# Kernel tuning notes

Measured on AMD Instinct MI355X. Metric: run time of the kernel, lower is better.

## Reference

```python
import jax, jax.numpy as jnp
import numpy as np

SEQ, B, I, H = 512, 64, 1024, 1024

def setup_inputs() -> dict:
    key = jax.random.key(0)
    ks = jax.random.split(key, 6)
    scale_ih = 1.0 / np.sqrt(I)
    scale_hh = 1.0 / np.sqrt(H)
    return {
        "input": jax.random.normal(ks[0], (SEQ, B, I), dtype=jnp.float32),
        "h_0": jax.random.normal(ks[1], (1, B, H), dtype=jnp.float32),
        "weight_ih": jax.random.normal(ks[2], (3 * H, I), dtype=jnp.float32) * scale_ih,
        "weight_hh": jax.random.normal(ks[3], (3 * H, H), dtype=jnp.float32) * scale_hh,
        "bias_ih": jax.random.normal(ks[4], (3 * H,), dtype=jnp.float32) * scale_hh,
        "bias_hh": jax.random.normal(ks[5], (3 * H,), dtype=jnp.float32) * scale_hh,
    }


def _gru_lbr0(input, h0, weight_ih, weight_hh, bias_ih, bias_hh):
    """Unidirectional GRU, ONNX linear_before_reset=0 semantics.

    r_t = sigmoid(x W_ir^T + b_ir + h W_hr^T + b_hr)
    z_t = sigmoid(x W_iz^T + b_iz + h W_hz^T + b_hz)
    n_t = tanh(x W_in^T + b_in + (r_t * h) W_hn^T + b_hn)
    h_t = (1 - z_t) * n_t + z_t * h
    """
    hidden = h0.shape[-1]
    # Precompute all input projections in one big GEMM: (S, B, 3H)
    gx = jnp.einsum('sbi,gi->sbg', input, weight_ih) + bias_ih
    W_hr, W_hz, W_hn = jnp.split(weight_hh, 3, axis=0)
    b_hr, b_hz, b_hn = jnp.split(bias_hh, 3, axis=0)

    def step(h, gx_t):
        gx_r, gx_z, gx_n = jnp.split(gx_t, 3, axis=-1)
        r = jax.nn.sigmoid(gx_r + h @ W_hr.T + b_hr)
        z = jax.nn.sigmoid(gx_z + h @ W_hz.T + b_hz)
        n = jnp.tanh(gx_n + (r * h) @ W_hn.T + b_hn)
        h_new = (1.0 - z) * n + z * h
        return h_new, h_new

    h_n, outputs = jax.lax.scan(step, h0, gx)
    return outputs, h_n  # (S, B, H), (B, H)


def reference(input, h_0, weight_ih, weight_hh, bias_ih, bias_hh):
    seq_len, batch, _ = input.shape
    hidden = weight_hh.shape[1]
    outputs, h_n = _gru_lbr0(input, h_0[0], weight_ih, weight_hh, bias_ih, bias_hh)
    # Match GRUWrapper output layout: Y = (S, num_dir=1, B, H), Y_h = (1, B, H)
    Y = outputs.reshape(seq_len, batch, 1, hidden).transpose(0, 2, 1, 3)
    Y_h = h_n[None, :, :]
    return (Y, Y_h)
```

## Files before the change

### kernel.cpp

```cpp
#include <hip/hip_runtime.h>

typedef unsigned short ushort_t;
typedef short sh8 __attribute__((ext_vector_type(8)));
typedef float f32x4 __attribute__((ext_vector_type(4)));

#define MFMA16(a,b,c) __builtin_amdgcn_mfma_f32_16x16x32_bf16((a),(b),(c),0,0,0)

#define SEQL   512
#define BATCH  64
#define HDIM   1024
#define G3     3072
#define AROWS  (SEQL*BATCH)
#define YSZ    (SEQL*BATCH*HDIM)
#define BH     (BATCH*HDIM)
#define NWG    64
#define NGEMM  192
#define NTILE  768

#define TILES_TOTAL (256*24)
#define TILES_PER_WG (TILES_TOTAL/NGEMM)

__device__ __forceinline__ ushort_t f2bf(float x) {
  unsigned u = __float_as_uint(x);
  u += 0x7FFFu + ((u >> 16) & 1u);
  return (ushort_t)(u >> 16);
}
__device__ __forceinline__ float bf2f(ushort_t h) {
  return __uint_as_float(((unsigned)h) << 16);
}

__global__ void cvt_kernel(const float* __restrict__ wih, const float* __restrict__ whh,
                           const float* __restrict__ h0,
                           ushort_t* __restrict__ WihH, ushort_t* __restrict__ WihL,
                           ushort_t* __restrict__ WhhH, ushort_t* __restrict__ WhhL,
                           ushort_t* __restrict__ hH) {
  const int NW = G3 * HDIM;
  int i0 = blockIdx.x * blockDim.x + threadIdx.x;
  int stride = gridDim.x * blockDim.x;
  for (int i = i0; i < NW; i += stride) {
    float x = wih[i]; ushort_t h = f2bf(x);
    WihH[i] = h; WihL[i] = f2bf(x - bf2f(h));
    float y = whh[i]; ushort_t g = f2bf(y);
    WhhH[i] = g; WhhL[i] = f2bf(y - bf2f(g));
  }
  for (int i = i0; i < BH; i += stride) {
    hH[i] = f2bf(h0[i]);
  }
}

__device__ __forceinline__ void gbar_flat(unsigned* slots, int g, int tid, unsigned e) {
  __syncthreads();
  if (tid < 64) {
    if (tid == 0)
      __hip_atomic_store(slots + g * 32, e, __ATOMIC_RELEASE, __HIP_MEMORY_SCOPE_AGENT);
    unsigned* sp = slots + tid * 32;
    while (__hip_atomic_load(sp, __ATOMIC_RELAXED, __HIP_MEMORY_SCOPE_AGENT) < e)
      __builtin_amdgcn_s_sleep(1);
    (void)__hip_atomic_load(sp, __ATOMIC_ACQUIRE, __HIP_MEMORY_SCOPE_AGENT);
  }
  __syncthreads();
}

__global__ __launch_bounds__(256, 1) void mega(
    const float* __restrict__ A,
    const ushort_t* __restrict__ WihH, const ushort_t* __restrict__ WihL,
    const float* __restrict__ bih,
    float* __restrict__ gx,
    const ushort_t* __restrict__ WhhH, const ushort_t* __restrict__ WhhL,
    const float* __restrict__ bhh,
    const float* __restrict__ h0f,
    ushort_t* __restrict__ hH,
    ushort_t* __restrict__ rhH,
    float* __restrict__ Y, float* __restrict__ Yh,
    unsigned* __restrict__ slots,
    unsigned* __restrict__ prog)
{
  extern __shared__ char lds[];
  const int g = blockIdx.x;
  const int tid = threadIdx.x;
  const int w = tid >> 6, l = tid & 63;
  const int lr = l & 15, lk = (l >> 4) * 8, rb = (l >> 4) * 4;

  if (g >= NWG) {
    const int base = g - NWG;
    for (int kk = 0; kk < TILES_PER_WG; ++kk) {
      int tile = base + NGEMM * kk;
      int mt = tile / 24, nt = tile % 24;

      f32x4 acc[2][8];
      #pragma unroll
      for (int mi = 0; mi < 2; ++mi)
        #pragma unroll
        for (int ni = 0; ni < 8; ++ni) acc[mi][ni] = (f32x4){0.f, 0.f, 0.f, 0.f};

      int arow0 = mt * 128 + w * 32 + lr;
      int brow0 = nt * 128 + lr;

      for (int k0 = 0; k0 < HDIM; k0 += 32) {
        int ka = k0 + lk;
        sh8 aH[2], aL[2];
        #pragma unroll
        for (int mi = 0; mi < 2; ++mi) {
          const float* ap = A + (size_t)(arow0 + mi * 16) * HDIM + ka;
          float4 x0 = *(const float4*)ap;
          float4 x1 = *(const float4*)(ap + 4);
          float xs[8] = {x0.x, x0.y, x0.z, x0.w, x1.x, x1.y, x1.z, x1.w};
          #pragma unroll
          for (int j = 0; j < 8; ++j) {
            ushort_t h = f2bf(xs[j]);
            aH[mi][j] = (short)h;
            aL[mi][j] = (short)f2bf(xs[j] - bf2f(h));
          }
        }
        #pragma unroll
        for (int ni = 0; ni < 8; ++ni) {
          const ushort_t* bh = WihH + (size_t)(brow0 + ni * 16) * HDIM + ka;
          const ushort_t* bl = WihL + (size_t)(brow0 + ni * 16) * HDIM + ka;
          sh8 bHf = *(const sh8*)bh;
          sh8 bLf = *(const sh8*)bl;
          #pragma unroll
          for (int mi = 0; mi < 2; ++mi) {
            acc[mi][ni] = MFMA16(aH[mi], bHf, acc[mi][ni]);
            acc[mi][ni] = MFMA16(aH[mi], bLf, acc[mi][ni]);
            acc[mi][ni] = MFMA16(aL[mi], bHf, acc[mi][ni]);
          }
        }
      }
      int rbq = (l >> 4) * 4;
      #pragma unroll
      for (int mi = 0; mi < 2; ++mi)
        #pragma unroll
        for (int ni = 0; ni < 8; ++ni) {
          int col = nt * 128 + ni * 16 + lr;
          float b = bih[col];
          #pragma unroll
          for (int j = 0; j < 4; ++j) {
            int row = mt * 128 + w * 32 + mi * 16 + rbq + j;
            __builtin_nontemporal_store(acc[mi][ni][j] + b, &gx[(size_t)row * G3 + col]);
          }
        }
      __syncthreads();
      if (tid == 0)
        __hip_atomic_fetch_add(prog + mt, 1u, __ATOMIC_RELEASE, __HIP_MEMORY_SCOPE_AGENT);
    }
    return;
  }

  const int c0 = g * 16, m0 = w * 16;
  const int c = c0 + lr;

  #pragma unroll
  for (int p = 0; p < 32; ++p) {
    int q = tid + p * 256;
    int flat = q * 16;
    int lrow = flat >> 11;
    int off = flat & 2047;
    int dst = flat ^ ((lrow & 7) << 4);
    const ushort_t* src;
    if (lrow < 16)      src = WhhH + (size_t)(c0 + lrow) * HDIM;
    else if (lrow < 32) src = WhhH + (size_t)(1024 + c0 + lrow - 16) * HDIM;
    else if (lrow < 48) src = WhhH + (size_t)(2048 + c0 + lrow - 32) * HDIM;
    else                src = WhhL + (size_t)(2048 + c0 + lrow - 48) * HDIM;
    *(sh8*)(lds + dst) = *(const sh8*)(src + (off >> 1));
  }
  __syncthreads();

  const float br = bhh[c], bz = bhh[1024 + c], bn = bhh[2048 + c];
  unsigned bar = 0;
  int pready = 0;

  float hold[4];
  #pragma unroll
  for (int j = 0; j < 4; ++j) hold[j] = h0f[(m0 + rb + j) * HDIM + c];

  {
    while (__hip_atomic_load(prog, __ATOMIC_RELAXED, __HIP_MEMORY_SCOPE_AGENT) < 24u)
      __builtin_amdgcn_s_sleep(1);
    (void)__hip_atomic_load(prog, __ATOMIC_ACQUIRE, __HIP_MEMORY_SCOPE_AGENT);
    pready = 1;
  }
  float gxr[4], gxz[4], gxn[4];
  #pragma unroll
  for (int j = 0; j < 4; ++j) {
    int b = m0 + rb + j;
    gxr[j] = __builtin_nontemporal_load(gx + (size_t)b * G3 + c);
    gxz[j] = __builtin_nontemporal_load(gx + (size_t)b * G3 + 1024 + c);
    gxn[j] = __builtin_nontemporal_load(gx + (size_t)b * G3 + 2048 + c);
  }

  for (int t = 0; t < SEQL; ++t) {
    const int par = t & 1;

    const ushort_t* ha = hH + par * BH + (size_t)(m0 + lr) * HDIM + lk;
    sh8 bufa[32];
    #pragma unroll
    for (int i = 0; i < 32; ++i) bufa[i] = *(const sh8*)(ha + i * 32);

    f32x4 accR = (f32x4){0,0,0,0}, accZ = (f32x4){0,0,0,0};
    #pragma unroll
    for (int i = 0; i < 32; ++i) {
      int byt = ((lr << 11) + ((i * 32 + lk) << 1)) ^ ((lr & 7) << 4);
      sh8 rW = *(const sh8*)(lds + byt);
      sh8 zW = *(const sh8*)(lds + 32768 + byt);
      accR = MFMA16(bufa[i], rW, accR);
      accZ = MFMA16(bufa[i], zW, accZ);
    }

    float zreg[4];
    #pragma unroll
    for (int j = 0; j < 4; ++j) {
      int b = m0 + rb + j;
      float pr = accR[j] + gxr[j] + br;
      float pz = accZ[j] + gxz[j] + bz;
      float r = 1.f / (1.f + __expf(-pr));
      zreg[j] = 1.f / (1.f + __expf(-pz));
      rhH[b * HDIM + c] = f2bf(r * hold[j]);
    }
    ++bar;
    gbar_flat(slots, g, tid, bar);

    const ushort_t* ra = rhH + (size_t)(m0 + lr) * HDIM + lk;
    #pragma unroll
    for (int i = 0; i < 32; ++i) bufa[i] = *(const sh8*)(ra + i * 32);

    int tn = (t + 1 < SEQL) ? t + 1 : t;
    {
      int blk = tn >> 1;
      if (blk >= pready) {
        while (__hip_atomic_load(prog + blk, __ATOMIC_RELAXED, __HIP_MEMORY_SCOPE_AGENT) < 24u)
          __builtin_amdgcn_s_sleep(1);
        (void)__hip_atomic_load(prog + blk, __ATOMIC_ACQUIRE, __HIP_MEMORY_SCOPE_AGENT);
        pready = blk + 1;
      }
      const float* gxn2 = gx + (size_t)tn * (BATCH * G3);
      #pragma unroll
      for (int j = 0; j < 4; ++j) {
        int b = m0 + rb + j;
        gxr[j] = __builtin_nontemporal_load(gxn2 + (size_t)b * G3 + c);
        gxz[j] = __builtin_nontemporal_load(gxn2 + (size_t)b * G3 + 1024 + c);
      }
    }

    f32x4 accN = (f32x4){0,0,0,0};
    #pragma unroll
    for (int i = 0; i < 32; ++i) {
      int byt = ((lr << 11) + ((i * 32 + lk) << 1)) ^ ((lr & 7) << 4);
      sh8 nW = *(const sh8*)(lds + 65536 + byt);
      sh8 nLo = *(const sh8*)(lds + 98304 + byt);
      accN = MFMA16(bufa[i], nW, accN);
      accN = MFMA16(bufa[i], nLo, accN);
    }

    ushort_t* hHn = hH + (par ^ 1) * BH;
    float gxnN[4];
    {
      const float* gxn2 = gx + (size_t)tn * (BATCH * G3);
      #pragma unroll
      for (int j = 0; j < 4; ++j) {
        int b = m0 + rb + j;
        gxnN[j] = __builtin_nontemporal_load(gxn2 + (size_t)b * G3 + 2048 + c);
      }
    }
    #pragma unroll
    for (int j = 0; j < 4; ++j) {
      int b = m0 + rb + j;
      float pn = accN[j] + gxn[j] + bn;
      float n = tanhf(pn);
      float z = zreg[j];
      float hnew = (1.f - z) * n + z * hold[j];
      hold[j] = hnew;
      __builtin_nontemporal_store(hnew, &Y[(size_t)t * BH + b * HDIM + c]);
      hHn[b * HDIM + c] = f2bf(hnew);
      if (t == SEQL - 1) __builtin_nontemporal_store(hnew, &Yh[b * HDIM + c]);
    }
    #pragma unroll
    for (int j = 0; j < 4; ++j) gxn[j] = gxnN[j];

    if (t < SEQL - 1) {
      ++bar;
      gbar_flat(slots, g, tid, bar);
    }
  }
}

extern "C" void kernel_launch(void* const* d_in, const int* in_sizes, int n_in,
                              void* d_out, int out_size, void* d_ws, size_t ws_size,
                              hipStream_t stream) {
  const float* input = (const float*)d_in[0];
  const float* h0    = (const float*)d_in[1];
  const float* wih   = (const float*)d_in[2];
  const float* whh   = (const float*)d_in[3];
  const float* bih   = (const float*)d_in[4];
  const float* bhh   = (const float*)d_in[5];

  char* ws = (char*)d_ws;
  size_t o = 0;
  float* gx = (float*)(ws + o);         o += (size_t)AROWS * G3 * 4;
  ushort_t* WihH = (ushort_t*)(ws + o); o += (size_t)G3 * HDIM * 2;
  ushort_t* WihL = (ushort_t*)(ws + o); o += (size_t)G3 * HDIM * 2;
  ushort_t* WhhH = (ushort_t*)(ws + o); o += (size_t)G3 * HDIM * 2;
  ushort_t* WhhL = (ushort_t*)(ws + o); o += (size_t)G3 * HDIM * 2;
  ushort_t* hH = (ushort_t*)(ws + o);   o += 2 * (size_t)BH * 2;
  ushort_t* rhH = (ushort_t*)(ws + o);  o += (size_t)BH * 2;
  unsigned* slots = (unsigned*)(ws + o); o += (size_t)NWG * 128;
  unsigned* prog = (unsigned*)(ws + o);  o += 256 * 4;

  float* Y  = (float*)d_out;
  float* Yh = (float*)d_out + (size_t)YSZ;

  (void)hipFuncSetAttribute((const void*)mega,
                            hipFuncAttributeMaxDynamicSharedMemorySize, 131072);

  (void)hipMemsetAsync(slots, 0, (size_t)NWG * 128 + 256 * 4, stream);
  cvt_kernel<<<2048, 256, 0, stream>>>(wih, whh, h0, WihH, WihL, WhhH, WhhL, hH);
  mega<<<NWG + NGEMM, 256, 131072, stream>>>(input, WihH, WihL, bih, gx,
                                             WhhH, WhhL, bhh, h0, hH, rhH,
                                             Y, Yh, slots, prog);
}
```

Measured before the change: 8.682 ms.

## Convert W_hh in-kernel during LDS staging and pace GEMM producers behind recurrence

Drops the separate bf16 hi/lo conversion of the recurrent weight matrix from the pre-pass and instead converts fp32 W_hh straight into LDS while the recurrence workgroups load their weight slice. This removes a full read/write pass over W_hh and two workspace buffers. It also adds pacing so the input-projection GEMM workgroups wait on the recurrence barrier counters before running too far ahead. The intent is to cut contention for memory bandwidth and cache with the latency-bound recurrent loop, at the cost of possibly stalling GEMM workers.

```diff
diff --git a/kernel.cpp b/kernel.cpp
--- a/kernel.cpp
+++ b/kernel.cpp
@@ -15,8 +15,6 @@
 #define BH     (BATCH*HDIM)
 #define NWG    64
 #define NGEMM  192
-#define NTILE  768
-
 #define TILES_TOTAL (256*24)
 #define TILES_PER_WG (TILES_TOTAL/NGEMM)
 
@@ -29,10 +27,8 @@
   return __uint_as_float(((unsigned)h) << 16);
 }
 
-__global__ void cvt_kernel(const float* __restrict__ wih, const float* __restrict__ whh,
-                           const float* __restrict__ h0,
+__global__ void cvt_kernel(const float* __restrict__ wih, const float* __restrict__ h0,
                            ushort_t* __restrict__ WihH, ushort_t* __restrict__ WihL,
-                           ushort_t* __restrict__ WhhH, ushort_t* __restrict__ WhhL,
                            ushort_t* __restrict__ hH) {
   const int NW = G3 * HDIM;
   int i0 = blockIdx.x * blockDim.x + threadIdx.x;
@@ -40,8 +36,6 @@
   for (int i = i0; i < NW; i += stride) {
     float x = wih[i]; ushort_t h = f2bf(x);
     WihH[i] = h; WihL[i] = f2bf(x - bf2f(h));
-    float y = whh[i]; ushort_t g = f2bf(y);
-    WhhH[i] = g; WhhL[i] = f2bf(y - bf2f(g));
   }
   for (int i = i0; i < BH; i += stride) {
     hH[i] = f2bf(h0[i]);
@@ -66,7 +60,7 @@
     const ushort_t* __restrict__ WihH, const ushort_t* __restrict__ WihL,
     const float* __restrict__ bih,
     float* __restrict__ gx,
-    const ushort_t* __restrict__ WhhH, const ushort_t* __restrict__ WhhL,
+    const float* __restrict__ whh,
     const float* __restrict__ bhh,
     const float* __restrict__ h0f,
     ushort_t* __restrict__ hH,
@@ -83,9 +77,16 @@
 
   if (g >= NWG) {
     const int base = g - NWG;
+    unsigned* pace = slots + (base & 63) * 32;
     for (int kk = 0; kk < TILES_PER_WG; ++kk) {
       int tile = base + NGEMM * kk;
       int mt = tile / 24, nt = tile % 24;
+
+      int emin = 2 * (mt - 31);
+      if (emin > 0) {
+        while ((int)__hip_atomic_load(pace, __ATOMIC_RELAXED, __HIP_MEMORY_SCOPE_AGENT) < emin)
+          __builtin_amdgcn_s_sleep(8);
+      }
 
       f32x4 acc[2][8];
       #pragma unroll
@@ -126,7 +127,6 @@
           }
         }
       }
-      int rbq = (l >> 4) * 4;
       #pragma unroll
       for (int mi = 0; mi < 2; ++mi)
         #pragma unroll
@@ -135,7 +135,7 @@
           float b = bih[col];
           #pragma unroll
           for (int j = 0; j < 4; ++j) {
-            int row = mt * 128 + w * 32 + mi * 16 + rbq + j;
+            int row = mt * 128 + w * 32 + mi * 16 + rb + j;
             __builtin_nontemporal_store(acc[mi][ni][j] + b, &gx[(size_t)row * G3 + col]);
           }
         }
@@ -156,12 +156,23 @@
     int lrow = flat >> 11;
     int off = flat & 2047;
     int dst = flat ^ ((lrow & 7) << 4);
-    const ushort_t* src;
-    if (lrow < 16)      src = WhhH + (size_t)(c0 + lrow) * HDIM;
-    else if (lrow < 32) src = WhhH + (size_t)(1024 + c0 + lrow - 16) * HDIM;
-    else if (lrow < 48) src = WhhH + (size_t)(2048 + c0 + lrow - 32) * HDIM;
-    else                src = WhhL + (size_t)(2048 + c0 + lrow - 48) * HDIM;
-    *(sh8*)(lds + dst) = *(const sh8*)(src + (off >> 1));
+    int col = off >> 1;
+    const float* src;
+    bool lo = false;
+    if (lrow < 16)      src = whh + (size_t)(c0 + lrow) * HDIM + col;
+    else if (lrow < 32) src = whh + (size_t)(1024 + c0 + lrow - 16) * HDIM + col;
+    else if (lrow < 48) src = whh + (size_t)(2048 + c0 + lrow - 32) * HDIM + col;
+    else              { src = whh + (size_t)(2048 + c0 + lrow - 48) * HDIM + col; lo = true; }
+    float4 x0 = *(const float4*)src;
+    float4 x1 = *(const float4*)(src + 4);
+    float xs[8] = {x0.x, x0.y, x0.z, x0.w, x1.x, x1.y, x1.z, x1.w};
+    union { ushort_t v[8]; sh8 s; } pk;
+    #pragma unroll
+    for (int j = 0; j < 8; ++j) {
+      ushort_t hi = f2bf(xs[j]);
+      pk.v[j] = lo ? f2bf(xs[j] - bf2f(hi)) : hi;
+    }
+    *(sh8*)(lds + dst) = pk.s;
   }
   __syncthreads();
 
@@ -298,8 +309,6 @@
   float* gx = (float*)(ws + o);         o += (size_t)AROWS * G3 * 4;
   ushort_t* WihH = (ushort_t*)(ws + o); o += (size_t)G3 * HDIM * 2;
   ushort_t* WihL = (ushort_t*)(ws + o); o += (size_t)G3 * HDIM * 2;
-  ushort_t* WhhH = (ushort_t*)(ws + o); o += (size_t)G3 * HDIM * 2;
-  ushort_t* WhhL = (ushort_t*)(ws + o); o += (size_t)G3 * HDIM * 2;
   ushort_t* hH = (ushort_t*)(ws + o);   o += 2 * (size_t)BH * 2;
   ushort_t* rhH = (ushort_t*)(ws + o);  o += (size_t)BH * 2;
   unsigned* slots = (unsigned*)(ws + o); o += (size_t)NWG * 128;
@@ -312,8 +321,8 @@
                             hipFuncAttributeMaxDynamicSharedMemorySize, 131072);
 
   (void)hipMemsetAsync(slots, 0, (size_t)NWG * 128 + 256 * 4, stream);
-  cvt_kernel<<<2048, 256, 0, stream>>>(wih, whh, h0, WihH, WihL, WhhH, WhhL, hH);
+  cvt_kernel<<<2048, 256, 0, stream>>>(wih, h0, WihH, WihL, hH);
   mega<<<NWG + NGEMM, 256, 131072, stream>>>(input, WihH, WihL, bih, gx,
-                                             WhhH, WhhL, bhh, h0, hH, rhH,
+                                             whh, bhh, h0, hH, rhH,
                                              Y, Yh, slots, prog);
 }
```

New measurement: 8.772 ms. Within noise of the previous version (+1.0%).
